# Kernel optimization log

Measured on AMD Instinct MI355X. Metric: run time of the kernel, lower is better.

## Reference

```python
import jax, jax.numpy as jnp
import numpy as np
from jax import lax

B, L, T = 64, 512, 52  # batch, seq_len, tag_size = target_size + 2


def setup_inputs() -> dict:
    key = jax.random.key(0)
    kf, kt, kl = jax.random.split(key, 3)
    feats = jax.random.normal(kf, (B, L, T), jnp.float32)
    transitions = jax.random.normal(kt, (T, T), jnp.float32) * 0.1
    # __init__ constraints: nothing transitions INTO start tag, nothing OUT of end tag
    transitions = transitions.at[:, T - 2].set(-1000.0).at[T - 1, :].set(-1000.0)
    lengths = jax.random.randint(kl, (B,), L // 2, L + 1)
    mask = (jnp.arange(L)[None, :] < lengths[:, None]).astype(jnp.int32)
    return {"feats": feats, "mask": mask, "transitions": transitions}


def reference(feats, mask, transitions):
    Bv, Lv, Tv = feats.shape
    START, END = Tv - 2, Tv - 1
    # absorb node potentials into edge potentials: scores[t,b,i,j] = feats[b,t,j] + trans[i,j]
    scores = feats.transpose(1, 0, 2)[:, :, None, :] + transitions[None, None, :, :]  # [L,B,T,T]
    lengths = mask.sum(axis=1)            # [B]
    mask_t = mask.T                       # [L,B]
    bidx = jnp.arange(Bv)

    partition0 = scores[0, :, START, :]   # [B,T]

    def step(partition, xs):
        sc, m = xs                        # sc: [B,T,T], m: [B]
        cur = sc + partition[:, :, None]  # max-plus transition
        new_p = cur.max(axis=1)           # [B,T]
        bp = jnp.argmax(cur, axis=1)      # [B,T]
        bp = jnp.where(m[:, None] > 0, bp, 0)  # zero backpointers at padded steps
        return new_p, (new_p, bp)

    _, (parts, bps) = lax.scan(step, partition0, (scores[1:], mask_t[1:]))
    hist = jnp.concatenate([partition0[None], parts], axis=0)      # [L,B,T]

    last_partition = hist[lengths - 1, bidx]                       # [B,T] value at last valid step
    last_values = last_partition[:, :, None] + transitions[None]   # [B,T,T]
    last_bp = jnp.argmax(last_values, axis=1)                      # [B,T]
    pointer0 = last_bp[:, END]                                     # [B] best tag at last position

    back = jnp.concatenate([bps, jnp.zeros((1, Bv, Tv), bps.dtype)], axis=0)  # [L,B,T]
    # insert the final pointer row at each sequence's last valid timestep
    back = back.at[lengths - 1, bidx, :].set(jnp.broadcast_to(pointer0[:, None], (Bv, Tv)))

    def back_step(ptr, bp_t):
        new_ptr = bp_t[bidx, ptr]
        return new_ptr, new_ptr

    _, rev = lax.scan(back_step, pointer0, back[:-1], reverse=True)  # rev[t] = tag at step t
    decode = jnp.concatenate([rev, pointer0[None]], axis=0)          # [L,B]
    return decode.T                                                  # [B,L]
```

## Files before the change

### kernel.cpp

```cpp
#include <hip/hip_runtime.h>

#define BB 64
#define LL 512
#define TT 52
#define START_TAG 50
#define END_TAG 51

__device__ __forceinline__ void lds_barrier() {
    __asm__ __volatile__("s_waitcnt lgkmcnt(0)\n\ts_barrier" ::: "memory");
}

__launch_bounds__(256, 1)
__global__ void viterbi_kernel(const float* __restrict__ feats,
                               const int* __restrict__ mask,
                               const float* __restrict__ trans,
                               int* __restrict__ out) {
    const int b    = blockIdx.x;
    const int tid  = threadIdx.x;
    const int lane = tid & 63;
    const int w    = tid >> 6;
    const int wbase = w * 13;

    __shared__ unsigned long long s_part[2][64 * 5 + 8];
    __shared__ unsigned char s_bp[LL * TT];
    __shared__ int s_tags[LL];

    int partial = 0;
    const int* mrow = mask + b * LL;
    #pragma unroll
    for (int k = 0; k < LL / 64; ++k) partial += mrow[lane + 64 * k];
    #pragma unroll
    for (int off = 32; off >= 1; off >>= 1) partial += __shfl_xor(partial, off, 64);
    const int n = partial;

    float creg[13];
    #pragma unroll
    for (int q = 0; q < 13; ++q)
        creg[q] = (lane < TT) ? trans[(wbase + q) * TT + lane] : 0.0f;
    const float tE = (lane < TT) ? trans[lane * TT + END_TAG] : 0.0f;

    const float* frow = feats + (size_t)b * LL * TT;

    float bestP = (lane < TT) ? (frow[lane] + trans[START_TAG * TT + lane]) : -3.0e38f;

    #pragma unroll
    for (int k = 0; k < LL / 256; ++k) s_tags[tid + 256 * k] = 0;

    const int slot = lane * 5 + w;

    auto step = [&](int t, int buf, float f) {
        float pv[13];
        #pragma unroll
        for (int q = 0; q < 13; ++q)
            pv[q] = __int_as_float(__builtin_amdgcn_readlane(__float_as_int(bestP), wbase + q));

        float bv[13]; int bq[13];
        #pragma unroll
        for (int q = 0; q < 13; ++q) { bv[q] = (f + creg[q]) + pv[q]; bq[q] = q; }
        #pragma unroll
        for (int s = 1; s < 13; s <<= 1) {
            #pragma unroll
            for (int i = 0; i + s < 13; i += 2 * s) {
                bool gt = bv[i + s] > bv[i];
                bv[i] = gt ? bv[i + s] : bv[i];
                bq[i] = gt ? bq[i + s] : bq[i];
            }
        }
        int pidx = wbase + bq[0];
        unsigned long long pk = ((unsigned long long)(unsigned)pidx << 32)
                              | (unsigned long long)(unsigned)__float_as_uint(bv[0]);
        s_part[buf][slot] = pk;
        lds_barrier();

        unsigned long long p0 = s_part[buf][lane * 5 + 0];
        unsigned long long p1 = s_part[buf][lane * 5 + 1];
        unsigned long long p2 = s_part[buf][lane * 5 + 2];
        unsigned long long p3 = s_part[buf][lane * 5 + 3];
        float cv = __uint_as_float((unsigned)p0); int ci = (int)(p0 >> 32);
        {
            float v1 = __uint_as_float((unsigned)p1); int i1 = (int)(p1 >> 32);
            bool gt = v1 > cv; cv = gt ? v1 : cv; ci = gt ? i1 : ci;
            float v2 = __uint_as_float((unsigned)p2); int i2 = (int)(p2 >> 32);
            gt = v2 > cv; cv = gt ? v2 : cv; ci = gt ? i2 : ci;
            float v3 = __uint_as_float((unsigned)p3); int i3 = (int)(p3 >> 32);
            gt = v3 > cv; cv = gt ? v3 : cv; ci = gt ? i3 : ci;
        }
        bestP = cv;
        if (tid < TT) s_bp[t * TT + tid] = (unsigned char)ci;
    };

    float fr[4];
    #pragma unroll
    for (int d = 0; d < 4; ++d) {
        int tt = 1 + d; if (tt > LL - 1) tt = LL - 1;
        fr[d] = (lane < TT) ? frow[tt * TT + lane] : 0.0f;
    }

    int t = 1;
    for (; t + 3 < n; t += 4) {
        #pragma unroll
        for (int d = 0; d < 4; ++d) {
            float f = fr[d];
            int tt = t + d + 4; if (tt > LL - 1) tt = LL - 1;
            fr[d] = (lane < TT) ? frow[tt * TT + lane] : 0.0f;
            step(t + d, d & 1, f);
        }
    }
    for (int d = 0; t < n; ++t, ++d) {
        step(t, d & 1, fr[d]);
    }

    float lv = (lane < TT) ? (bestP + tE) : -3.0e38f;
    int li = lane;
    #pragma unroll
    for (int off = 32; off >= 1; off >>= 1) {
        float ov = __shfl_xor(lv, off, 64);
        int   oi = __shfl_xor(li, off, 64);
        if (ov > lv || (ov == lv && oi < li)) { lv = ov; li = oi; }
    }
    const int ptr0 = li;

    __syncthreads();
    if (tid == 0) {
        s_tags[n - 1] = ptr0;
        s_tags[LL - 1] = ptr0;
        int ptr = ptr0;
        for (int tt = n - 2; tt >= 0; --tt) {
            ptr = s_bp[(tt + 1) * TT + ptr];
            s_tags[tt] = ptr;
        }
    }
    __syncthreads();

    int* orow = out + b * LL;
    #pragma unroll
    for (int k = 0; k < LL / 256; ++k) orow[tid + 256 * k] = s_tags[tid + 256 * k];
}

extern "C" void kernel_launch(void* const* d_in, const int* in_sizes, int n_in,
                              void* d_out, int out_size, void* d_ws, size_t ws_size,
                              hipStream_t stream) {
    const float* feats = (const float*)d_in[0];
    const int*   mask  = (const int*)d_in[1];
    const float* trans = (const float*)d_in[2];
    int* out = (int*)d_out;
    viterbi_kernel<<<dim3(BB), dim3(256), 0, stream>>>(feats, mask, trans, out);
}
```

Baseline: 293.2 us.

## Parallelize Viterbi backtrace via segment maps and use max-then-index argmax

The serial single-thread backtrace is split into 8 segments. The segments are handled in three phases: all 52 start tags per segment are traced in parallel to build composition maps, one thread chains the segment entry tags, and then 8 threads walk their segments to write tags. Separately, the per-step argmax now computes the max with fmaxf first and then takes the lowest index whose bits equal the max, packing an equality flag into an unsigned min. This replaces compare-select chains. The result is a shorter serial backtrace at the cost of extra LDS traffic and barriers, and tie-breaking now picks the first index.

After: 289.9 us. About the same (-1.1%).

```diff
diff --git a/kernel.cpp b/kernel.cpp
--- a/kernel.cpp
+++ b/kernel.cpp
@@ -9,6 +9,8 @@
 __device__ __forceinline__ void lds_barrier() {
     __asm__ __volatile__("s_waitcnt lgkmcnt(0)\n\ts_barrier" ::: "memory");
 }
+
+__device__ __forceinline__ unsigned umin32(unsigned a, unsigned b) { return a < b ? a : b; }
 
 __launch_bounds__(256, 1)
 __global__ void viterbi_kernel(const float* __restrict__ feats,
@@ -24,6 +26,8 @@
     __shared__ unsigned long long s_part[2][64 * 5 + 8];
     __shared__ unsigned char s_bp[LL * TT];
     __shared__ int s_tags[LL];
+    __shared__ unsigned char s_map[8 * 52];
+    __shared__ int s_ent[8];
 
     int partial = 0;
     const int* mrow = mask + b * LL;
@@ -49,26 +53,39 @@
     const int slot = lane * 5 + w;
 
     auto step = [&](int t, int buf, float f) {
-        float pv[13];
+        float tmp[13];
         #pragma unroll
-        for (int q = 0; q < 13; ++q)
-            pv[q] = __int_as_float(__builtin_amdgcn_readlane(__float_as_int(bestP), wbase + q));
+        for (int q = 0; q < 13; ++q) tmp[q] = f + creg[q];
 
-        float bv[13]; int bq[13];
+        float bv[13];
         #pragma unroll
-        for (int q = 0; q < 13; ++q) { bv[q] = (f + creg[q]) + pv[q]; bq[q] = q; }
+        for (int q = 0; q < 13; ++q) {
+            float pq = __int_as_float(__builtin_amdgcn_readlane(__float_as_int(bestP), wbase + q));
+            bv[q] = tmp[q] + pq;
+        }
+
+        float m0 = fmaxf(fmaxf(bv[0], bv[1]), bv[2]);
+        float m1 = fmaxf(fmaxf(bv[3], bv[4]), bv[5]);
+        float m2 = fmaxf(fmaxf(bv[6], bv[7]), bv[8]);
+        float m3 = fmaxf(fmaxf(bv[9], bv[10]), bv[11]);
+        float M  = fmaxf(fmaxf(fmaxf(m0, m1), fmaxf(m2, m3)), bv[12]);
+
+        unsigned kk[13];
         #pragma unroll
-        for (int s = 1; s < 13; s <<= 1) {
-            #pragma unroll
-            for (int i = 0; i + s < 13; i += 2 * s) {
-                bool gt = bv[i + s] > bv[i];
-                bv[i] = gt ? bv[i + s] : bv[i];
-                bq[i] = gt ? bq[i + s] : bq[i];
-            }
+        for (int q = 0; q < 13; ++q) {
+            unsigned e  = __float_as_uint(bv[q]) ^ __float_as_uint(M);
+            unsigned nz = umin32(e, 1u);
+            kk[q] = (nz << 6) | (unsigned)q;
         }
-        int pidx = wbase + bq[0];
-        unsigned long long pk = ((unsigned long long)(unsigned)pidx << 32)
-                              | (unsigned long long)(unsigned)__float_as_uint(bv[0]);
+        unsigned k0 = umin32(umin32(kk[0], kk[1]), kk[2]);
+        unsigned k1 = umin32(umin32(kk[3], kk[4]), kk[5]);
+        unsigned k2 = umin32(umin32(kk[6], kk[7]), kk[8]);
+        unsigned k3 = umin32(umin32(kk[9], kk[10]), kk[11]);
+        unsigned km = umin32(umin32(umin32(k0, k1), umin32(k2, k3)), kk[12]);
+        unsigned pidx = (unsigned)wbase + (km & 63u);
+
+        unsigned long long pk = ((unsigned long long)pidx << 32)
+                              | (unsigned long long)__float_as_uint(M);
         s_part[buf][slot] = pk;
         lds_barrier();
 
@@ -76,15 +93,18 @@
         unsigned long long p1 = s_part[buf][lane * 5 + 1];
         unsigned long long p2 = s_part[buf][lane * 5 + 2];
         unsigned long long p3 = s_part[buf][lane * 5 + 3];
-        float cv = __uint_as_float((unsigned)p0); int ci = (int)(p0 >> 32);
-        {
-            float v1 = __uint_as_float((unsigned)p1); int i1 = (int)(p1 >> 32);
-            bool gt = v1 > cv; cv = gt ? v1 : cv; ci = gt ? i1 : ci;
-            float v2 = __uint_as_float((unsigned)p2); int i2 = (int)(p2 >> 32);
-            gt = v2 > cv; cv = gt ? v2 : cv; ci = gt ? i2 : ci;
-            float v3 = __uint_as_float((unsigned)p3); int i3 = (int)(p3 >> 32);
-            gt = v3 > cv; cv = gt ? v3 : cv; ci = gt ? i3 : ci;
-        }
+        float v0 = __uint_as_float((unsigned)p0);
+        float v1 = __uint_as_float((unsigned)p1);
+        float v2 = __uint_as_float((unsigned)p2);
+        float v3 = __uint_as_float((unsigned)p3);
+        float cv = fmaxf(fmaxf(v0, v1), fmaxf(v2, v3));
+        unsigned cb = __float_as_uint(cv);
+        unsigned c0 = (umin32(__float_as_uint(v0) ^ cb, 1u) << 6) | (unsigned)(p0 >> 32);
+        unsigned c1 = (umin32(__float_as_uint(v1) ^ cb, 1u) << 6) | (unsigned)(p1 >> 32);
+        unsigned c2 = (umin32(__float_as_uint(v2) ^ cb, 1u) << 6) | (unsigned)(p2 >> 32);
+        unsigned c3 = (umin32(__float_as_uint(v3) ^ cb, 1u) << 6) | (unsigned)(p3 >> 32);
+        unsigned ci = umin32(umin32(c0, c1), umin32(c2, c3)) & 63u;
+
         bestP = cv;
         if (tid < TT) s_bp[t * TT + tid] = (unsigned char)ci;
     };
@@ -106,9 +126,7 @@
             step(t + d, d & 1, f);
         }
     }
-    for (int d = 0; t < n; ++t, ++d) {
-        step(t, d & 1, fr[d]);
-    }
+    for (int d = 0; t < n; ++t, ++d) step(t, d & 1, fr[d]);
 
     float lv = (lane < TT) ? (bestP + tE) : -3.0e38f;
     int li = lane;
@@ -121,13 +139,42 @@
     const int ptr0 = li;
 
     __syncthreads();
+
+    const int W  = n - 1;
+    const int Sc = (W + 7) >> 3;
+    {
+        int v0 = tid;
+        int k0 = v0 / 52, y0 = v0 - k0 * 52;
+        int v1 = tid + 256;
+        bool a1 = (v1 < 416);
+        int k1 = a1 ? v1 / 52 : 7, y1 = a1 ? (v1 - k1 * 52) : 0;
+        int s0a = k0 * Sc, s1a = min(s0a + Sc, W);
+        int s0b = k1 * Sc, s1b = min(s0b + Sc, W);
+        int xa = y0, xb = y1;
+        for (int s = 0; s < Sc; ++s) {
+            int ga = s0a + s, gb = s0b + s;
+            if (ga < s1a) xa = s_bp[(n - 1 - ga) * TT + xa];
+            if (gb < s1b) xb = s_bp[(n - 1 - gb) * TT + xb];
+        }
+        s_map[k0 * 52 + y0] = (unsigned char)xa;
+        if (a1) s_map[k1 * 52 + y1] = (unsigned char)xb;
+    }
+    __syncthreads();
     if (tid == 0) {
+        int e = ptr0; s_ent[0] = e;
+        #pragma unroll
+        for (int k = 1; k < 8; ++k) { e = s_map[(k - 1) * 52 + e]; s_ent[k] = e; }
         s_tags[n - 1] = ptr0;
         s_tags[LL - 1] = ptr0;
-        int ptr = ptr0;
-        for (int tt = n - 2; tt >= 0; --tt) {
-            ptr = s_bp[(tt + 1) * TT + ptr];
-            s_tags[tt] = ptr;
+    }
+    __syncthreads();
+    if (tid < 8) {
+        int k = tid;
+        int x = s_ent[k];
+        int ss0 = k * Sc, ss1 = min(ss0 + Sc, W);
+        for (int s = ss0; s < ss1; ++s) {
+            x = s_bp[(n - 1 - s) * TT + x];
+            s_tags[n - 2 - s] = x;
         }
     }
     __syncthreads();
```
